# Kernel tuning notes

Measured on AMD Instinct MI355X. Metric: run time of the kernel, lower is better.

## Reference

```python
import jax, jax.numpy as jnp
import numpy as np

B, T, D, HS = 4, 4096, 1024, 64

def setup_inputs() -> dict:
    key = jax.random.key(0)
    kx, kq, kk, kv = jax.random.split(key, 4)
    s = 1.0 / np.sqrt(D)  # torch Linear default-ish init scale
    return {
        "x": jax.random.normal(kx, (B, T, D), dtype=jnp.float32),
        "Wq": jax.random.uniform(kq, (D, HS), jnp.float32, -s, s),
        "Wk": jax.random.uniform(kk, (D, HS), jnp.float32, -s, s),
        "Wv": jax.random.uniform(kv, (D, HS), jnp.float32, -s, s),
    }

def reference(x, Wq, Wk, Wv):
    # x: [B,T,D]; Wq/Wk/Wv: [D,HS]
    q = jnp.einsum('btd,dh->bth', x, Wq)
    k = jnp.einsum('btd,dh->bth', x, Wk)
    v = jnp.einsum('btd,dh->bth', x, Wv)
    # NOTE: source scales by C**-0.5 with C = d_model (input dim), not head_size
    scale = jnp.asarray(D, x.dtype) ** -0.5
    weights = jnp.einsum('bqh,bkh->bqk', q, k) * scale  # [B,T,T]
    weights = jax.nn.softmax(weights, axis=-1)
    out = jnp.einsum('bqk,bkh->bqh', weights, v)  # [B,T,HS]
    return out
```

## Files before the change

### kernel.cpp

```cpp
#include <hip/hip_runtime.h>


typedef __bf16 bf16;
typedef __bf16 bf16x4 __attribute__((ext_vector_type(4)));
typedef __bf16 bf16x8 __attribute__((ext_vector_type(8)));
typedef float  f32x16 __attribute__((ext_vector_type(16)));

#define MFMA(a, b, c) __builtin_amdgcn_mfma_f32_32x32x16_bf16(a, b, c, 0, 0, 0)

constexpr int T = 4096, D = 1024, HS = 64;
constexpr int ROWS = 4 * T;
constexpr float QSCL = 0.045084220027797f;

__device__ __forceinline__ void gld16(const void* g, void* l) {
    __builtin_amdgcn_global_load_lds(
        (const __attribute__((address_space(1))) unsigned int*)g,
        (__attribute__((address_space(3))) unsigned int*)l, 16, 0, 0);
}

__device__ inline f32x16 zero16() {
    f32x16 z;
#pragma unroll
    for (int i = 0; i < 16; ++i) z[i] = 0.f;
    return z;
}

__global__ __launch_bounds__(256) void prep_wt(
    const float* __restrict__ Wq, const float* __restrict__ Wk,
    const float* __restrict__ Wv, bf16* __restrict__ Wt)
{
    __shared__ float Xf[64 * 68];
    const int m = blockIdx.x >> 4, dt = blockIdx.x & 15;
    const float* W = (m == 0) ? Wq : ((m == 1) ? Wk : Wv);
    const int d0 = dt * 64;
#pragma unroll
    for (int j = 0; j < 4; ++j) {
        int i = threadIdx.x + 256 * j;
        int dr = i >> 4, c4 = i & 15;
        float4 v = *(const float4*)(W + (size_t)(d0 + dr) * 64 + c4 * 4);
        *(float4*)&Xf[dr * 68 + c4 * 4] = v;
    }
    __syncthreads();
    const float scl = (m == 0) ? QSCL : 1.0f;
#pragma unroll
    for (int j = 0; j < 4; ++j) {
        int o = threadIdx.x + 256 * j;
        int h = o >> 4, dc = o & 15;
        bf16x4 w;
#pragma unroll
        for (int k = 0; k < 4; ++k) w[k] = (bf16)(Xf[(dc * 4 + k) * 68 + h] * scl);
        *(bf16x4*)(Wt + (size_t)(m * 64 + h) * D + d0 + dc * 4) = w;
    }
}

__global__ __launch_bounds__(256, 1) void qkv_proj(
    const float* __restrict__ x, const bf16* __restrict__ Wt,
    bf16* __restrict__ Qg, bf16* __restrict__ Kgt, bf16* __restrict__ Vgt)
{
    __shared__ __align__(16) float Xs[64 * 64];
    __shared__ __align__(16) short Ws[192 * 64];
    const int tid = threadIdx.x;
    const int w = tid >> 6, lane = tid & 63, ln5 = lane & 31, hi = lane >> 5;
    const int tt = w & 1, hh = w >> 1;
    const int r0 = blockIdx.x * 64;
    const int wb = tid & 448;

    f32x16 accQ = zero16(), accK = zero16(), accV = zero16();
    const int rx  = tt * 32 + ln5;
    const int hq  = hh * 32 + ln5;
    const int swz = ln5 & 7;

    for (int kc = 0; kc < 16; ++kc) {
        __syncthreads();
#pragma unroll
        for (int k2 = 0; k2 < 4; ++k2) {
            int s = k2 * 256 + tid;
            int r = s >> 4, j = s & 15, u = j ^ (r & 15);
            gld16(x + (size_t)(r0 + r) * D + kc * 64 + u * 4,
                  &Xs[(k2 * 256 + wb) * 4]);
        }
#pragma unroll
        for (int k2 = 0; k2 < 6; ++k2) {
            int s = k2 * 256 + tid;
            int h = s >> 3, j = s & 7, u = j ^ (h & 7);
            gld16(Wt + (size_t)h * D + kc * 64 + u * 8,
                  &Ws[(k2 * 256 + wb) * 8]);
        }
        __syncthreads();

        bf16x8 fx[4];
#pragma unroll
        for (int ks = 0; ks < 4; ++ks) {
            int u0 = ks * 4 + hi * 2;
            float4 a = *(const float4*)&Xs[rx * 64 + ((u0)     ^ (rx & 15)) * 4];
            float4 b = *(const float4*)&Xs[rx * 64 + ((u0 + 1) ^ (rx & 15)) * 4];
            bf16x8 f;
            f[0] = (bf16)a.x; f[1] = (bf16)a.y; f[2] = (bf16)a.z; f[3] = (bf16)a.w;
            f[4] = (bf16)b.x; f[5] = (bf16)b.y; f[6] = (bf16)b.z; f[7] = (bf16)b.w;
            fx[ks] = f;
        }
#pragma unroll
        for (int ks = 0; ks < 4; ++ks) {
            int j = ((ks * 2 + hi) ^ swz) * 8;
            bf16x8 aq = *(const bf16x8*)&Ws[(hq)       * 64 + j];
            bf16x8 ak = *(const bf16x8*)&Ws[(hq + 64)  * 64 + j];
            bf16x8 bv = *(const bf16x8*)&Ws[(hq + 128) * 64 + j];
            accQ = MFMA(aq, fx[ks], accQ);
            accK = MFMA(ak, fx[ks], accK);
            accV = MFMA(fx[ks], bv, accV);
        }
    }

    {
        int t = r0 + tt * 32 + ln5;
#pragma unroll
        for (int g = 0; g < 4; ++g) {
            int h0 = hh * 32 + 8 * g + 4 * hi;
            bf16x4 vq, vk;
#pragma unroll
            for (int k = 0; k < 4; ++k) { vq[k] = (bf16)accQ[4*g+k]; vk[k] = (bf16)accK[4*g+k]; }
            *(bf16x4*)(Qg + (size_t)t * HS + h0) = vq;
            int j = (h0 >> 3) ^ (t & 7);
            *(bf16x4*)(Kgt + (size_t)t * HS + j * 8 + 4 * hi) = vk;
        }
        int hr = hh * 32 + ln5;
#pragma unroll
        for (int g = 0; g < 4; ++g) {
            int t0 = tt * 32 + 8 * g + 4 * hi;
            bf16x4 vv;
#pragma unroll
            for (int k = 0; k < 4; ++k) vv[k] = (bf16)accV[4*g+k];
            int j = (t0 >> 3) ^ (hr & 7);
            *(bf16x4*)(Vgt + (size_t)blockIdx.x * 4096 + hr * 64 + j * 8 + 4 * hi) = vv;
        }
    }
}

__global__ __launch_bounds__(256, 2) void attn(
    const bf16* __restrict__ Qg, const bf16* __restrict__ Kgt,
    const bf16* __restrict__ Vgt, float* __restrict__ Op,
    float* __restrict__ Lp, float* __restrict__ out, int split)
{
    __shared__ __align__(16) short KV[16384];
    __shared__ __align__(16) short Ps[4][32 * 72];
    __shared__ float Lx[128];

    const int tid = threadIdx.x;
    const int w = tid >> 6, lane = tid & 63, ln5 = lane & 31, hi = lane >> 5;
    const int wq = w & 1, wk = w >> 1;
    const int wb = tid & 448;

    int b, qt, half;
    if (split == 2)      { int c2 = blockIdx.x & 7;  b = c2 >> 1; half = c2 & 1; qt = blockIdx.x >> 3; }
    else if (split == 4) { int c2 = blockIdx.x & 15; b = c2 >> 2; half = c2 & 3; qt = blockIdx.x >> 4; }
    else                 { b = blockIdx.x & 3; half = 0; qt = blockIdx.x >> 2; }
    const int rbase = b * T;
    const int seg = T / split;
    const int kb0 = rbase + half * seg;
    const int nc = seg / 128;
    const int qrow = rbase + qt * 64 + wq * 32 + ln5;

    const bf16* qp = Qg + (size_t)qrow * HS + hi * 8;
    bf16x8 bq[4];
#pragma unroll
    for (int ks = 0; ks < 4; ++ks) bq[ks] = *(const bf16x8*)(qp + ks * 16);

    f32x16 O0 = zero16(), O1 = zero16();
    float l = 0.f;
    short* Pw = &Ps[w][0];
    const int swz = ln5 & 7;
    const int krow0 = wk * 4096 + ln5 * 64;
    const int krow1 = wk * 4096 + (32 + ln5) * 64;
    const int vrow0 = 8192 + wk * 4096 + ln5 * 64;
    const int vrow1 = 8192 + wk * 4096 + (32 + ln5) * 64;
    const bf16* Kc = Kgt + (size_t)kb0 * HS;
    const bf16* Vc = Vgt + (size_t)kb0 * HS;

    for (int c = 0; c < nc; ++c) {
        __syncthreads();
#pragma unroll
        for (int k2 = 0; k2 < 4; ++k2) {
            int s = k2 * 256 + tid;
            gld16(Kc + (size_t)c * 8192 + s * 8, &KV[(k2 * 256 + wb) * 8]);
            gld16(Vc + (size_t)c * 8192 + s * 8, &KV[8192 + (k2 * 256 + wb) * 8]);
        }
        __syncthreads();

        f32x16 S0 = zero16(), S1 = zero16();
#pragma unroll
        for (int ks = 0; ks < 4; ++ks) {
            int j = ((ks * 2 + hi) ^ swz) * 8;
            bf16x8 a0 = *(const bf16x8*)&KV[krow0 + j];
            bf16x8 a1 = *(const bf16x8*)&KV[krow1 + j];
            S0 = MFMA(a0, bq[ks], S0);
            S1 = MFMA(a1, bq[ks], S1);
        }

#pragma unroll
        for (int g = 0; g < 4; ++g) {
            float p0 = __builtin_amdgcn_exp2f(S0[4 * g + 0]);
            float p1 = __builtin_amdgcn_exp2f(S0[4 * g + 1]);
            float p2 = __builtin_amdgcn_exp2f(S0[4 * g + 2]);
            float p3 = __builtin_amdgcn_exp2f(S0[4 * g + 3]);
            l += (p0 + p1) + (p2 + p3);
            bf16x4 pv; pv[0] = (bf16)p0; pv[1] = (bf16)p1; pv[2] = (bf16)p2; pv[3] = (bf16)p3;
            *(bf16x4*)&Pw[ln5 * 72 + 8 * g + 4 * hi] = pv;
        }
#pragma unroll
        for (int g = 0; g < 4; ++g) {
            float p0 = __builtin_amdgcn_exp2f(S1[4 * g + 0]);
            float p1 = __builtin_amdgcn_exp2f(S1[4 * g + 1]);
            float p2 = __builtin_amdgcn_exp2f(S1[4 * g + 2]);
            float p3 = __builtin_amdgcn_exp2f(S1[4 * g + 3]);
            l += (p0 + p1) + (p2 + p3);
            bf16x4 pv; pv[0] = (bf16)p0; pv[1] = (bf16)p1; pv[2] = (bf16)p2; pv[3] = (bf16)p3;
            *(bf16x4*)&Pw[ln5 * 72 + 32 + 8 * g + 4 * hi] = pv;
        }

#pragma unroll
        for (int ks = 0; ks < 4; ++ks) {
            int j = ((ks * 2 + hi) ^ swz) * 8;
            bf16x8 bp = *(const bf16x8*)&Pw[ln5 * 72 + ks * 16 + hi * 8];
            bf16x8 v0 = *(const bf16x8*)&KV[vrow0 + j];
            bf16x8 v1 = *(const bf16x8*)&KV[vrow1 + j];
            O0 = MFMA(v0, bp, O0);
            O1 = MFMA(v1, bp, O1);
        }
    }

    l += __shfl_xor(l, 32, 64);
    __syncthreads();

    float* Ox = (float*)&KV[0];
    if (wk == 1) {
#pragma unroll
        for (int r = 0; r < 16; ++r) Ox[(wq * 32 + r) * 64 + lane] = O0[r];
#pragma unroll
        for (int r = 0; r < 16; ++r) Ox[(wq * 32 + 16 + r) * 64 + lane] = O1[r];
        Lx[wq * 64 + lane] = l;
    }
    __syncthreads();
    if (wk == 0) {
#pragma unroll
        for (int r = 0; r < 16; ++r) O0[r] += Ox[(wq * 32 + r) * 64 + lane];
#pragma unroll
        for (int r = 0; r < 16; ++r) O1[r] += Ox[(wq * 32 + 16 + r) * 64 + lane];
        l += Lx[wq * 64 + lane];
        if (split == 1) {
            float inv = 1.0f / l;
#pragma unroll
            for (int g = 0; g < 4; ++g) {
                float4 o;
                o.x = O0[4*g+0] * inv; o.y = O0[4*g+1] * inv;
                o.z = O0[4*g+2] * inv; o.w = O0[4*g+3] * inv;
                *(float4*)(out + (size_t)qrow * HS + 8 * g + 4 * hi) = o;
            }
#pragma unroll
            for (int g = 0; g < 4; ++g) {
                float4 o;
                o.x = O1[4*g+0] * inv; o.y = O1[4*g+1] * inv;
                o.z = O1[4*g+2] * inv; o.w = O1[4*g+3] * inv;
                *(float4*)(out + (size_t)qrow * HS + 32 + 8 * g + 4 * hi) = o;
            }
        } else {
            float* Od = Op + (size_t)half * ROWS * HS + (size_t)qrow * HS;
#pragma unroll
            for (int g = 0; g < 4; ++g) {
                float4 o;
                o.x = O0[4*g+0]; o.y = O0[4*g+1]; o.z = O0[4*g+2]; o.w = O0[4*g+3];
                *(float4*)(Od + 8 * g + 4 * hi) = o;
            }
#pragma unroll
            for (int g = 0; g < 4; ++g) {
                float4 o;
                o.x = O1[4*g+0]; o.y = O1[4*g+1]; o.z = O1[4*g+2]; o.w = O1[4*g+3];
                *(float4*)(Od + 32 + 8 * g + 4 * hi) = o;
            }
            if (hi == 0) Lp[half * ROWS + qrow] = l;
        }
    }
}

__global__ __launch_bounds__(256) void attn_reduce(
    const float* __restrict__ Op, const float* __restrict__ Lp,
    float* __restrict__ out, int split)
{
    int idx = blockIdx.x * 256 + threadIdx.x;
    int row = idx >> 4;
    float4 s; s.x = s.y = s.z = s.w = 0.f;
    float lsum = 0.f;
    for (int h = 0; h < split; ++h) {
        float4 a = *(const float4*)(Op + (size_t)h * ROWS * HS + (size_t)idx * 4);
        s.x += a.x; s.y += a.y; s.z += a.z; s.w += a.w;
        lsum += Lp[h * ROWS + row];
    }
    float inv = 1.0f / lsum;
    s.x *= inv; s.y *= inv; s.z *= inv; s.w *= inv;
    *(float4*)(out + (size_t)idx * 4) = s;
}

extern "C" void kernel_launch(void* const* d_in, const int* in_sizes, int n_in,
                              void* d_out, int out_size, void* d_ws, size_t ws_size,
                              hipStream_t stream)
{
    const float* x  = (const float*)d_in[0];
    const float* Wq = (const float*)d_in[1];
    const float* Wk = (const float*)d_in[2];
    const float* Wv = (const float*)d_in[3];
    float* out = (float*)d_out;

    char* ws = (char*)d_ws;
    bf16* Qg  = (bf16*)(ws);
    bf16* Kgt = (bf16*)(ws + ((size_t)2 << 20));
    bf16* Vgt = (bf16*)(ws + ((size_t)4 << 20));
    bf16* Wt  = (bf16*)(ws + ((size_t)6 << 20));
    float* Lp = (float*)(ws + ((size_t)6 << 20));
    float* Op = (float*)(ws + ((size_t)6 << 20) + ((size_t)1 << 19));

    const size_t base = ((size_t)6 << 20) + ((size_t)1 << 19);
    int split = 1;
    if (ws_size >= base + (size_t)4 * ROWS * HS * sizeof(float)) split = 4;
    else if (ws_size >= base + (size_t)2 * ROWS * HS * sizeof(float)) split = 2;

    prep_wt<<<48, 256, 0, stream>>>(Wq, Wk, Wv, Wt);
    qkv_proj<<<ROWS / 64, 256, 0, stream>>>(x, Wt, Qg, Kgt, Vgt);
    attn<<<256 * split, 256, 0, stream>>>(Qg, Kgt, Vgt, Op, Lp, out, split);
    if (split > 1)
        attn_reduce<<<(ROWS * HS / 4) / 256, 256, 0, stream>>>(Op, Lp, out, split);
}
```

Measured before the change: 154.2 us.

## Double-buffer qkv and attention loads, split projection per matrix, retile attention

qkv_proj now launches three times as many blocks, each computing only one of Q, K or V, with an XCD-aware row mapping and a double-buffered LDS pipeline so the next chunk loads while the current one computes. The attention kernel processes 128 query rows per block in 64-key chunks, double-buffers K/V in LDS, reuses each K fragment across two query tiles, and restructures the P·V split across waves. The block-to-(batch, split) mapping for split=4 is changed for locality. In exchange, the projection reads x three times, and the attention kernel holds more accumulators, which raises register pressure and halves the block count.

New measurement: 150.7 us. 1.02x faster.

```diff
diff --git a/kernel.cpp b/kernel.cpp
--- a/kernel.cpp
+++ b/kernel.cpp
@@ -53,85 +53,89 @@
     }
 }
 
-__global__ __launch_bounds__(256, 1) void qkv_proj(
+__global__ __launch_bounds__(256, 3) void qkv_proj(
     const float* __restrict__ x, const bf16* __restrict__ Wt,
     bf16* __restrict__ Qg, bf16* __restrict__ Kgt, bf16* __restrict__ Vgt)
 {
-    __shared__ __align__(16) float Xs[64 * 64];
-    __shared__ __align__(16) short Ws[192 * 64];
+    __shared__ __align__(16) float Xs[2][64 * 64];
+    __shared__ __align__(16) short Ws[2][64 * 64];
     const int tid = threadIdx.x;
     const int w = tid >> 6, lane = tid & 63, ln5 = lane & 31, hi = lane >> 5;
     const int tt = w & 1, hh = w >> 1;
-    const int r0 = blockIdx.x * 64;
+    const int xcd = blockIdx.x & 7, t3 = blockIdx.x >> 3;
+    const int which = t3 % 3, mlocal = t3 / 3;
+    const int r0 = (xcd * 32 + mlocal) * 64;
     const int wb = tid & 448;
 
-    f32x16 accQ = zero16(), accK = zero16(), accV = zero16();
-    const int rx  = tt * 32 + ln5;
-    const int hq  = hh * 32 + ln5;
-    const int swz = ln5 & 7;
-
-    for (int kc = 0; kc < 16; ++kc) {
-        __syncthreads();
+    auto stage = [&](int kc, int buf) {
 #pragma unroll
         for (int k2 = 0; k2 < 4; ++k2) {
             int s = k2 * 256 + tid;
             int r = s >> 4, j = s & 15, u = j ^ (r & 15);
             gld16(x + (size_t)(r0 + r) * D + kc * 64 + u * 4,
-                  &Xs[(k2 * 256 + wb) * 4]);
-        }
-#pragma unroll
-        for (int k2 = 0; k2 < 6; ++k2) {
+                  &Xs[buf][(k2 * 256 + wb) * 4]);
+        }
+#pragma unroll
+        for (int k2 = 0; k2 < 2; ++k2) {
             int s = k2 * 256 + tid;
             int h = s >> 3, j = s & 7, u = j ^ (h & 7);
-            gld16(Wt + (size_t)h * D + kc * 64 + u * 8,
-                  &Ws[(k2 * 256 + wb) * 8]);
-        }
-        __syncthreads();
-
-        bf16x8 fx[4];
+            gld16(Wt + (size_t)(which * 64 + h) * D + kc * 64 + u * 8,
+                  &Ws[buf][(k2 * 256 + wb) * 8]);
+        }
+    };
+
+    f32x16 acc = zero16();
+    const int rx = tt * 32 + ln5;
+    const int hq = hh * 32 + ln5;
+    const int swz = ln5 & 7;
+
+    stage(0, 0);
+    __syncthreads();
+    for (int kc = 0; kc < 16; ++kc) {
+        const int cur = kc & 1;
+        if (kc < 15) stage(kc + 1, cur ^ 1);
+        const float* Xb = &Xs[cur][0];
+        const short* Wb = &Ws[cur][0];
 #pragma unroll
         for (int ks = 0; ks < 4; ++ks) {
             int u0 = ks * 4 + hi * 2;
-            float4 a = *(const float4*)&Xs[rx * 64 + ((u0)     ^ (rx & 15)) * 4];
-            float4 b = *(const float4*)&Xs[rx * 64 + ((u0 + 1) ^ (rx & 15)) * 4];
-            bf16x8 f;
-            f[0] = (bf16)a.x; f[1] = (bf16)a.y; f[2] = (bf16)a.z; f[3] = (bf16)a.w;
-            f[4] = (bf16)b.x; f[5] = (bf16)b.y; f[6] = (bf16)b.z; f[7] = (bf16)b.w;
-            fx[ks] = f;
-        }
-#pragma unroll
-        for (int ks = 0; ks < 4; ++ks) {
-            int j = ((ks * 2 + hi) ^ swz) * 8;
-            bf16x8 aq = *(const bf16x8*)&Ws[(hq)       * 64 + j];
-            bf16x8 ak = *(const bf16x8*)&Ws[(hq + 64)  * 64 + j];
-            bf16x8 bv = *(const bf16x8*)&Ws[(hq + 128) * 64 + j];
-            accQ = MFMA(aq, fx[ks], accQ);
-            accK = MFMA(ak, fx[ks], accK);
-            accV = MFMA(fx[ks], bv, accV);
-        }
-    }
-
-    {
+            float4 a = *(const float4*)&Xb[rx * 64 + ((u0)     ^ (rx & 15)) * 4];
+            float4 b = *(const float4*)&Xb[rx * 64 + ((u0 + 1) ^ (rx & 15)) * 4];
+            bf16x8 fx;
+            fx[0] = (bf16)a.x; fx[1] = (bf16)a.y; fx[2] = (bf16)a.z; fx[3] = (bf16)a.w;
+            fx[4] = (bf16)b.x; fx[5] = (bf16)b.y; fx[6] = (bf16)b.z; fx[7] = (bf16)b.w;
+            bf16x8 wf = *(const bf16x8*)&Wb[hq * 64 + (((ks * 2 + hi) ^ swz) * 8)];
+            if (which < 2) acc = MFMA(wf, fx, acc);
+            else           acc = MFMA(fx, wf, acc);
+        }
+        __syncthreads();
+    }
+
+    if (which < 2) {
         int t = r0 + tt * 32 + ln5;
 #pragma unroll
         for (int g = 0; g < 4; ++g) {
             int h0 = hh * 32 + 8 * g + 4 * hi;
-            bf16x4 vq, vk;
-#pragma unroll
-            for (int k = 0; k < 4; ++k) { vq[k] = (bf16)accQ[4*g+k]; vk[k] = (bf16)accK[4*g+k]; }
-            *(bf16x4*)(Qg + (size_t)t * HS + h0) = vq;
-            int j = (h0 >> 3) ^ (t & 7);
-            *(bf16x4*)(Kgt + (size_t)t * HS + j * 8 + 4 * hi) = vk;
-        }
+            bf16x4 v;
+#pragma unroll
+            for (int k = 0; k < 4; ++k) v[k] = (bf16)acc[4 * g + k];
+            if (which == 0) {
+                *(bf16x4*)(Qg + (size_t)t * HS + h0) = v;
+            } else {
+                int j = (h0 >> 3) ^ (t & 7);
+                *(bf16x4*)(Kgt + (size_t)t * HS + j * 8 + 4 * hi) = v;
+            }
+        }
+    } else {
         int hr = hh * 32 + ln5;
 #pragma unroll
         for (int g = 0; g < 4; ++g) {
             int t0 = tt * 32 + 8 * g + 4 * hi;
-            bf16x4 vv;
-#pragma unroll
-            for (int k = 0; k < 4; ++k) vv[k] = (bf16)accV[4*g+k];
+            bf16x4 v;
+#pragma unroll
+            for (int k = 0; k < 4; ++k) v[k] = (bf16)acc[4 * g + k];
             int j = (t0 >> 3) ^ (hr & 7);
-            *(bf16x4*)(Vgt + (size_t)blockIdx.x * 4096 + hr * 64 + j * 8 + 4 * hi) = vv;
+            *(bf16x4*)(Vgt + (size_t)r0 * HS + hr * 64 + j * 8 + 4 * hi) = v;
         }
     }
 }
@@ -141,8 +145,8 @@
     const bf16* __restrict__ Vgt, float* __restrict__ Op,
     float* __restrict__ Lp, float* __restrict__ out, int split)
 {
-    __shared__ __align__(16) short KV[16384];
-    __shared__ __align__(16) short Ps[4][32 * 72];
+    __shared__ __align__(16) short KV[2][8192];
+    __shared__ __align__(16) short Ps[4][64 * 40];
     __shared__ float Lx[128];
 
     const int tid = threadIdx.x;
@@ -151,49 +155,62 @@
     const int wb = tid & 448;
 
     int b, qt, half;
-    if (split == 2)      { int c2 = blockIdx.x & 7;  b = c2 >> 1; half = c2 & 1; qt = blockIdx.x >> 3; }
-    else if (split == 4) { int c2 = blockIdx.x & 15; b = c2 >> 2; half = c2 & 3; qt = blockIdx.x >> 4; }
-    else                 { b = blockIdx.x & 3; half = 0; qt = blockIdx.x >> 2; }
+    if (split == 4) {
+        int rest = blockIdx.x >> 3; qt = rest & 31;
+        int combo = (blockIdx.x & 7) + 8 * (rest >> 5);
+        b = combo >> 2; half = combo & 3;
+    } else if (split == 2) {
+        int c2 = blockIdx.x & 7; b = c2 >> 1; half = c2 & 1; qt = blockIdx.x >> 3;
+    } else { b = blockIdx.x & 3; half = 0; qt = blockIdx.x >> 2; }
+
     const int rbase = b * T;
     const int seg = T / split;
     const int kb0 = rbase + half * seg;
-    const int nc = seg / 128;
-    const int qrow = rbase + qt * 64 + wq * 32 + ln5;
-
-    const bf16* qp = Qg + (size_t)qrow * HS + hi * 8;
-    bf16x8 bq[4];
-#pragma unroll
-    for (int ks = 0; ks < 4; ++ks) bq[ks] = *(const bf16x8*)(qp + ks * 16);
-
-    f32x16 O0 = zero16(), O1 = zero16();
-    float l = 0.f;
+    const int nc = seg / 64;
+    const int qrow0 = rbase + qt * 128 + wq * 64;
+
+    bf16x8 bq[2][4];
+    {
+        const bf16* qp = Qg + (size_t)(qrow0 + ln5) * HS + hi * 8;
+#pragma unroll
+        for (int qs = 0; qs < 2; ++qs)
+#pragma unroll
+            for (int ks = 0; ks < 4; ++ks)
+                bq[qs][ks] = *(const bf16x8*)(qp + (size_t)qs * 32 * HS + ks * 16);
+    }
+
+    const bf16* Kc = Kgt + (size_t)kb0 * HS;
+    const bf16* Vc = Vgt + (size_t)kb0 * HS;
+    auto stage = [&](int c, int buf) {
+#pragma unroll
+        for (int k2 = 0; k2 < 2; ++k2) {
+            int s = k2 * 256 + tid;
+            gld16(Kc + (size_t)c * 4096 + s * 8, &KV[buf][(k2 * 256 + wb) * 8]);
+            gld16(Vc + (size_t)c * 4096 + s * 8, &KV[buf][4096 + (k2 * 256 + wb) * 8]);
+        }
+    };
+
+    f32x16 O00 = zero16(), O01 = zero16(), O10 = zero16(), O11 = zero16();
+    float l0 = 0.f, l1 = 0.f;
     short* Pw = &Ps[w][0];
     const int swz = ln5 & 7;
-    const int krow0 = wk * 4096 + ln5 * 64;
-    const int krow1 = wk * 4096 + (32 + ln5) * 64;
-    const int vrow0 = 8192 + wk * 4096 + ln5 * 64;
-    const int vrow1 = 8192 + wk * 4096 + (32 + ln5) * 64;
-    const bf16* Kc = Kgt + (size_t)kb0 * HS;
-    const bf16* Vc = Vgt + (size_t)kb0 * HS;
+    const int krow = (wk * 32 + ln5) * 64;
+
+    stage(0, 0);
+    __syncthreads();
 
     for (int c = 0; c < nc; ++c) {
-        __syncthreads();
-#pragma unroll
-        for (int k2 = 0; k2 < 4; ++k2) {
-            int s = k2 * 256 + tid;
-            gld16(Kc + (size_t)c * 8192 + s * 8, &KV[(k2 * 256 + wb) * 8]);
-            gld16(Vc + (size_t)c * 8192 + s * 8, &KV[8192 + (k2 * 256 + wb) * 8]);
-        }
-        __syncthreads();
+        const int cur = c & 1;
+        if (c + 1 < nc) stage(c + 1, cur ^ 1);
+        const short* Kb = &KV[cur][0];
+        const short* Vb = &KV[cur][4096];
 
         f32x16 S0 = zero16(), S1 = zero16();
 #pragma unroll
         for (int ks = 0; ks < 4; ++ks) {
-            int j = ((ks * 2 + hi) ^ swz) * 8;
-            bf16x8 a0 = *(const bf16x8*)&KV[krow0 + j];
-            bf16x8 a1 = *(const bf16x8*)&KV[krow1 + j];
-            S0 = MFMA(a0, bq[ks], S0);
-            S1 = MFMA(a1, bq[ks], S1);
+            bf16x8 kf = *(const bf16x8*)&Kb[krow + (((ks * 2 + hi) ^ swz) * 8)];
+            S0 = MFMA(kf, bq[0][ks], S0);
+            S1 = MFMA(kf, bq[1][ks], S1);
         }
 
 #pragma unroll
@@ -202,9 +219,9 @@
             float p1 = __builtin_amdgcn_exp2f(S0[4 * g + 1]);
             float p2 = __builtin_amdgcn_exp2f(S0[4 * g + 2]);
             float p3 = __builtin_amdgcn_exp2f(S0[4 * g + 3]);
-            l += (p0 + p1) + (p2 + p3);
+            l0 += (p0 + p1) + (p2 + p3);
             bf16x4 pv; pv[0] = (bf16)p0; pv[1] = (bf16)p1; pv[2] = (bf16)p2; pv[3] = (bf16)p3;
-            *(bf16x4*)&Pw[ln5 * 72 + 8 * g + 4 * hi] = pv;
+            *(bf16x4*)&Pw[ln5 * 40 + 8 * g + 4 * hi] = pv;
         }
 #pragma unroll
         for (int g = 0; g < 4; ++g) {
@@ -212,71 +229,93 @@
             float p1 = __builtin_amdgcn_exp2f(S1[4 * g + 1]);
             float p2 = __builtin_amdgcn_exp2f(S1[4 * g + 2]);
             float p3 = __builtin_amdgcn_exp2f(S1[4 * g + 3]);
-            l += (p0 + p1) + (p2 + p3);
+            l1 += (p0 + p1) + (p2 + p3);
             bf16x4 pv; pv[0] = (bf16)p0; pv[1] = (bf16)p1; pv[2] = (bf16)p2; pv[3] = (bf16)p3;
-            *(bf16x4*)&Pw[ln5 * 72 + 32 + 8 * g + 4 * hi] = pv;
-        }
-
-#pragma unroll
-        for (int ks = 0; ks < 4; ++ks) {
-            int j = ((ks * 2 + hi) ^ swz) * 8;
-            bf16x8 bp = *(const bf16x8*)&Pw[ln5 * 72 + ks * 16 + hi * 8];
-            bf16x8 v0 = *(const bf16x8*)&KV[vrow0 + j];
-            bf16x8 v1 = *(const bf16x8*)&KV[vrow1 + j];
-            O0 = MFMA(v0, bp, O0);
-            O1 = MFMA(v1, bp, O1);
-        }
-    }
-
-    l += __shfl_xor(l, 32, 64);
-    __syncthreads();
-
-    float* Ox = (float*)&KV[0];
+            *(bf16x4*)&Pw[(32 + ln5) * 40 + 8 * g + 4 * hi] = pv;
+        }
+
+#pragma unroll
+        for (int ks = 0; ks < 2; ++ks) {
+            int ku = (wk * 4 + ks * 2 + hi) ^ swz;
+            bf16x8 pf0 = *(const bf16x8*)&Pw[ln5 * 40 + ks * 16 + hi * 8];
+            bf16x8 pf1 = *(const bf16x8*)&Pw[(32 + ln5) * 40 + ks * 16 + hi * 8];
+            bf16x8 vf0 = *(const bf16x8*)&Vb[ln5 * 64 + ku * 8];
+            bf16x8 vf1 = *(const bf16x8*)&Vb[(32 + ln5) * 64 + ku * 8];
+            O00 = MFMA(vf0, pf0, O00);
+            O01 = MFMA(vf0, pf1, O01);
+            O10 = MFMA(vf1, pf0, O10);
+            O11 = MFMA(vf1, pf1, O11);
+        }
+        __syncthreads();
+    }
+
+    l0 += __shfl_xor(l0, 32, 64);
+    l1 += __shfl_xor(l1, 32, 64);
+
+    float* Ox = (float*)&KV[0][0];
     if (wk == 1) {
 #pragma unroll
-        for (int r = 0; r < 16; ++r) Ox[(wq * 32 + r) * 64 + lane] = O0[r];
-#pragma unroll
-        for (int r = 0; r < 16; ++r) Ox[(wq * 32 + 16 + r) * 64 + lane] = O1[r];
-        Lx[wq * 64 + lane] = l;
+        for (int g = 0; g < 4; ++g)
+#pragma unroll
+            for (int k = 0; k < 4; ++k) {
+                int h0 = 8 * g + 4 * hi + k;
+                Ox[wq * 4096 + h0 * 64 + ln5]             = O00[4 * g + k];
+                Ox[wq * 4096 + h0 * 64 + 32 + ln5]        = O01[4 * g + k];
+                Ox[wq * 4096 + (32 + h0) * 64 + ln5]      = O10[4 * g + k];
+                Ox[wq * 4096 + (32 + h0) * 64 + 32 + ln5] = O11[4 * g + k];
+            }
+        if (hi == 0) { Lx[wq * 64 + ln5] = l0; Lx[wq * 64 + 32 + ln5] = l1; }
     }
     __syncthreads();
     if (wk == 0) {
 #pragma unroll
-        for (int r = 0; r < 16; ++r) O0[r] += Ox[(wq * 32 + r) * 64 + lane];
-#pragma unroll
-        for (int r = 0; r < 16; ++r) O1[r] += Ox[(wq * 32 + 16 + r) * 64 + lane];
-        l += Lx[wq * 64 + lane];
+        for (int g = 0; g < 4; ++g)
+#pragma unroll
+            for (int k = 0; k < 4; ++k) {
+                int h0 = 8 * g + 4 * hi + k;
+                O00[4 * g + k] += Ox[wq * 4096 + h0 * 64 + ln5];
+                O01[4 * g + k] += Ox[wq * 4096 + h0 * 64 + 32 + ln5];
+                O10[4 * g + k] += Ox[wq * 4096 + (32 + h0) * 64 + ln5];
+                O11[4 * g + k] += Ox[wq * 4096 + (32 + h0) * 64 + 32 + ln5];
+            }
+        l0 += Lx[wq * 64 + ln5];
+        l1 += Lx[wq * 64 + 32 + ln5];
+
+        int q0 = qrow0 + ln5, q1 = qrow0 + 32 + ln5;
         if (split == 1) {
-            float inv = 1.0f / l;
+            float i0 = 1.0f / l0, i1 = 1.0f / l1;
 #pragma unroll
             for (int g = 0; g < 4; ++g) {
+                int h0 = 8 * g + 4 * hi;
                 float4 o;
-                o.x = O0[4*g+0] * inv; o.y = O0[4*g+1] * inv;
-                o.z = O0[4*g+2] * inv; o.w = O0[4*g+3] * inv;
-                *(float4*)(out + (size_t)qrow * HS + 8 * g + 4 * hi) = o;
-            }
+                o.x = O00[4*g+0]*i0; o.y = O00[4*g+1]*i0; o.z = O00[4*g+2]*i0; o.w = O00[4*g+3]*i0;
+                *(float4*)(out + (size_t)q0 * HS + h0) = o;
+                o.x = O01[4*g+0]*i1; o.y = O01[4*g+1]*i1; o.z = O01[4*g+2]*i1; o.w = O01[4*g+3]*i1;
+                *(float4*)(out + (size_t)q1 * HS + h0) = o;
+                o.x = O10[4*g+0]*i0; o.y = O10[4*g+1]*i0; o.z = O10[4*g+2]*i0; o.w = O10[4*g+3]*i0;
+                *(float4*)(out + (size_t)q0 * HS + 32 + h0) = o;
+                o.x = O11[4*g+0]*i1; o.y = O11[4*g+1]*i1; o.z = O11[4*g+2]*i1; o.w = O11[4*g+3]*i1;
+                *(float4*)(out + (size_t)q1 * HS + 32 + h0) = o;
+            }
+        } else {
+            float* Od = Op + (size_t)half * ROWS * HS;
 #pragma unroll
             for (int g = 0; g < 4; ++g) {
+                int h0 = 8 * g + 4 * hi;
                 float4 o;
-                o.x = O1[4*g+0] * inv; o.y = O1[4*g+1] * inv;
-                o.z = O1[4*g+2] * inv; o.w = O1[4*g+3] * inv;
-                *(float4*)(out + (size_t)qrow * HS + 32 + 8 * g + 4 * hi) = o;
-            }
-        } else {
-            float* Od = Op + (size_t)half * ROWS * HS + (size_t)qrow * HS;
-#pragma unroll
-            for (int g = 0; g < 4; ++g) {
-                float4 o;
-                o.x = O0[4*g+0]; o.y = O0[4*g+1]; o.z = O0[4*g+2]; o.w = O0[4*g+3];
-                *(float4*)(Od + 8 * g + 4 * hi) = o;
-            }
-#pragma unroll
-            for (int g = 0; g < 4; ++g) {
-                float4 o;
-                o.x = O1[4*g+0]; o.y = O1[4*g+1]; o.z = O1[4*g+2]; o.w = O1[4*g+3];
-                *(float4*)(Od + 32 + 8 * g + 4 * hi) = o;
-            }
-            if (hi == 0) Lp[half * ROWS + qrow] = l;
+                o.x = O00[4*g+0]; o.y = O00[4*g+1]; o.z = O00[4*g+2]; o.w = O00[4*g+3];
+                *(float4*)(Od + (size_t)q0 * HS + h0) = o;
+                o.x = O01[4*g+0]; o.y = O01[4*g+1]; o.z = O01[4*g+2]; o.w = O01[4*g+3];
+                *(float4*)(Od + (size_t)q1 * HS + h0) = o;
+                o.x = O10[4*g+0]; o.y = O10[4*g+1]; o.z = O10[4*g+2]; o.w = O10[4*g+3];
+                *(float4*)(Od + (size_t)q0 * HS + 32 + h0) = o;
+                o.x = O11[4*g+0]; o.y = O11[4*g+1]; o.z = O11[4*g+2]; o.w = O11[4*g+3];
+                *(float4*)(Od + (size_t)q1 * HS + 32 + h0) = o;
+            }
+            if (hi == 0) {
+                Lp[half * ROWS + q0] = l0;
+                Lp[half * ROWS + q1] = l1;
+            }
         }
     }
 }
@@ -323,8 +362,8 @@
     else if (ws_size >= base + (size_t)2 * ROWS * HS * sizeof(float)) split = 2;
 
     prep_wt<<<48, 256, 0, stream>>>(Wq, Wk, Wv, Wt);
-    qkv_proj<<<ROWS / 64, 256, 0, stream>>>(x, Wt, Qg, Kgt, Vgt);
-    attn<<<256 * split, 256, 0, stream>>>(Qg, Kgt, Vgt, Op, Lp, out, split);
+    qkv_proj<<<768, 256, 0, stream>>>(x, Wt, Qg, Kgt, Vgt);
+    attn<<<128 * split, 256, 0, stream>>>(Qg, Kgt, Vgt, Op, Lp, out, split);
     if (split > 1)
         attn_reduce<<<(ROWS * HS / 4) / 256, 256, 0, stream>>>(Op, Lp, out, split);
 }
```
